# Kernel optimization log

Hardware: AMD Instinct MI355X
Metric: run time of the kernel (lower is better)

Reference implementation:

```python
import jax, jax.numpy as jnp
import numpy as np

# 4D convolution via lax.conv_general_dilated with 4 spatial dims.
# Layout: input (N, C, D, H, W, T), kernel (O, I, d, h, w, t).
DN = ('NCDHWT', 'OIDHWT', 'NCDHWT')


def conv4d(x, w, b, pad):
    # torch Conv2d/Conv4d is cross-correlation, matching lax.conv_general_dilated
    y = jax.lax.conv_general_dilated(
        x, w, window_strides=(1, 1, 1, 1),
        padding=[(pad, pad)] * 4, dimension_numbers=DN)
    return y + b.reshape(1, -1, 1, 1, 1, 1)


def _kaiming(key, shape):
    fan_out = shape[0] * int(np.prod(shape[2:]))
    std = np.sqrt(2.0 / fan_out)
    return (jax.random.normal(key, shape, dtype=jnp.float32) * std).astype(jnp.float32)


def setup_inputs() -> dict:
    key = jax.random.key(0)
    ks = jax.random.split(key, 11)
    B, W, H = 256, 16, 16
    corr = jax.random.normal(ks[0], (B, W * H, W, H), dtype=jnp.float32)
    w1 = _kaiming(ks[1], (1, 1, 17, 17, 9, 9))
    w2 = _kaiming(ks[2], (1, 1, 7, 7, 7, 7))
    w3 = _kaiming(ks[3], (1, 1, 5, 5, 5, 5))
    w4 = _kaiming(ks[4], (1, 1, 3, 3, 3, 3))
    w5 = _kaiming(ks[5], (1, 1, 8, 8, 1, 1))
    b1 = jax.random.normal(ks[6], (1,), dtype=jnp.float32) * 0.01
    b2 = jax.random.normal(ks[7], (1,), dtype=jnp.float32) * 0.01
    b3 = jax.random.normal(ks[8], (1,), dtype=jnp.float32) * 0.01
    b4 = jax.random.normal(ks[9], (1,), dtype=jnp.float32) * 0.01
    b5 = jax.random.normal(ks[10], (1,), dtype=jnp.float32) * 0.01
    return {"corr": corr, "w1": w1, "b1": b1, "w2": w2, "b2": b2,
            "w3": w3, "b3": b3, "w4": w4, "b4": b4, "w5": w5, "b5": b5}


def reference(corr, w1, b1, w2, b2, w3, b3, w4, b4, w5, b5):
    B, HW, W, H = corr.shape
    x = corr.reshape(B, 1, W, H, W, H)          # (B,1,16,16,16,16)
    x = jax.nn.relu(conv4d(x, w1, b1, 4))       # (B,1, 8, 8,16,16)
    x = jax.nn.relu(conv4d(x, w2, b2, 3))
    x = jax.nn.relu(conv4d(x, w3, b3, 2))
    x = jax.nn.relu(conv4d(x, w4, b4, 1))
    out = jax.nn.sigmoid(conv4d(x, w5, b5, 0))  # (B,1, 1, 1,16,16)
    return out.reshape(B, 1, W, H)
```

## Files before the change

### kernel.cpp

```cpp
#include <hip/hip_runtime.h>
#include <math.h>


typedef short bf16x8 __attribute__((ext_vector_type(8)));
typedef float f32x4 __attribute__((ext_vector_type(4)));
typedef unsigned int u32x4 __attribute__((ext_vector_type(4)));

#define XTS 72

__device__ __forceinline__ unsigned short f2bf(float f) {
  unsigned int u = __float_as_uint(f);
  u += 0x7fffu + ((u >> 16) & 1u);
  return (unsigned short)(u >> 16);
}

template <int KSZ, int PAD>
__device__ __forceinline__ void build_mid(const float* __restrict__ w,
                                          unsigned short* __restrict__ Bg, int gid) {
  const int lane = gid & 63;
  const int n_tile = (gid >> 6) & 3;
  const int chunk = (gid >> 8) & 1;
  const int tap = gid >> 9;
  const int kw = tap / KSZ, kt = tap - kw * KSZ;
  const int dh_o = n_tile * 16 + (lane & 15);
  const int d_o = dh_o >> 3, h_o = dh_o & 7;
  const int kbase = chunk * 32 + (lane >> 4) * 8;
  unsigned int pk[4];
#pragma unroll
  for (int p = 0; p < 4; ++p) {
    unsigned short half[2];
#pragma unroll
    for (int s = 0; s < 2; ++s) {
      const int k = kbase + p * 2 + s;
      const int d_i = k >> 3, h_i = k & 7;
      const int kd = d_i - d_o + PAD, kh = h_i - h_o + PAD;
      float v = 0.f;
      if (kd >= 0 && kd < KSZ && kh >= 0 && kh < KSZ)
        v = w[((kd * KSZ + kh) * KSZ + kw) * KSZ + kt];
      half[s] = f2bf(v);
    }
    pk[p] = (unsigned int)half[0] | ((unsigned int)half[1] << 16);
  }
  *(int4*)(Bg + (size_t)gid * 8) = make_int4(pk[0], pk[1], pk[2], pk[3]);
}

__global__ __launch_bounds__(256) void build_all(const float* __restrict__ w1,
                                                 const float* __restrict__ w2,
                                                 const float* __restrict__ w3,
                                                 const float* __restrict__ w4,
                                                 unsigned short* __restrict__ Bg1,
                                                 unsigned short* __restrict__ Bg2,
                                                 unsigned short* __restrict__ Bg3,
                                                 unsigned short* __restrict__ Bg4) {
  const int bid = blockIdx.x, tid = threadIdx.x;
  if (bid < 648) {
    const int gid = bid * 256 + tid;
    const int lane = gid & 63;
    const int n_tile = (gid >> 6) & 3;
    const int chunk = (gid >> 8) & 7;
    const int kwkt = gid >> 11;
    const int kw = kwkt / 9, kt = kwkt - kw * 9;
    const int dh_o = n_tile * 16 + (lane & 15);
    const int d_o = dh_o >> 3, h_o = dh_o & 7;
    const int kbase = chunk * 32 + (lane >> 4) * 8;
    unsigned int pk[4];
#pragma unroll
    for (int p = 0; p < 4; ++p) {
      unsigned short half[2];
#pragma unroll
      for (int s = 0; s < 2; ++s) {
        const int k = kbase + p * 2 + s;
        const int d_i = k >> 4, h_i = k & 15;
        const int kd = d_i - d_o + 4, kh = h_i - h_o + 4;
        float v = 0.f;
        if (kd >= 0 && kd < 17 && kh >= 0 && kh < 17)
          v = w1[((kd * 17 + kh) * 9 + kw) * 9 + kt];
        half[s] = f2bf(v);
      }
      pk[p] = (unsigned int)half[0] | ((unsigned int)half[1] << 16);
    }
    *(int4*)(Bg1 + (size_t)gid * 8) = make_int4(pk[0], pk[1], pk[2], pk[3]);
  } else if (bid < 746) {
    build_mid<7, 3>(w2, Bg2, (bid - 648) * 256 + tid);
  } else if (bid < 796) {
    build_mid<5, 2>(w3, Bg3, (bid - 746) * 256 + tid);
  } else {
    build_mid<3, 1>(w4, Bg4, (bid - 796) * 256 + tid);
  }
}

__device__ __forceinline__ void l1_load_tap(const unsigned short* XT,
                                            const unsigned short* __restrict__ Bg,
                                            int chbase, int kwkt, int wave, int lane,
                                            int quad, int tl, bf16x8 (&A)[8], bf16x8 (&B)[8]) {
  const int kw = kwkt / 9, kt = kwkt - kw * 9;
  const int t_i = tl + kt - 4;
  const bool tv = (unsigned)t_i < 16u;
  int ro[4];
#pragma unroll
  for (int m = 0; m < 4; ++m) {
    const int w_i = wave * 4 + m + kw - 4;
    const bool v = tv && ((unsigned)w_i < 16u);
    const int row = v ? (w_i * 16 + t_i) : 256;
    ro[m] = row * XTS + quad * 8;
  }
#pragma unroll
  for (int c = 0; c < 2; ++c)
#pragma unroll
    for (int m = 0; m < 4; ++m)
      A[c * 4 + m] = *(const bf16x8*)&XT[ro[m] + c * 32];
#pragma unroll
  for (int c = 0; c < 2; ++c)
#pragma unroll
    for (int n = 0; n < 4; ++n)
      B[c * 4 + n] = *(const bf16x8*)(Bg + (((size_t)(kwkt * 8 + chbase + c) * 4 + n) << 9) +
                                      lane * 8);
}

__device__ __forceinline__ void mfma16(const bf16x8 (&A)[8], const bf16x8 (&B)[8],
                                       f32x4 (&acc)[4][4]) {
#pragma unroll
  for (int c = 0; c < 2; ++c)
#pragma unroll
    for (int m = 0; m < 4; ++m)
#pragma unroll
      for (int n = 0; n < 4; ++n)
        acc[m][n] = __builtin_amdgcn_mfma_f32_16x16x32_bf16(A[c * 4 + m], B[c * 4 + n],
                                                            acc[m][n], 0, 0, 0);
}

__global__ __launch_bounds__(256) void conv_l1_mfma(const float* __restrict__ x,
                                                    const unsigned short* __restrict__ Bg,
                                                    float* __restrict__ P) {
  __shared__ __align__(16) unsigned short XT[257 * XTS];
  const int bx = blockIdx.x;
  const int b = bx >> 1, khalf = bx & 1;
  const int tid = threadIdx.x;
  const int lane = tid & 63, wave = tid >> 6;
  const int quad = lane >> 4, tl = lane & 15;
  const float* xb = x + (size_t)b * 65536;
  f32x4 acc[4][4] = {};

  if (tid < 9) *(int4*)&XT[256 * XTS + tid * 8] = make_int4(0, 0, 0, 0);

  for (int qq = 0; qq < 2; ++qq) {
    const int q = khalf * 2 + qq;
    __syncthreads();
#pragma unroll
    for (int it = 0; it < 8; ++it) {
      const int i = tid + it * 256;
      const int dhp = i >> 6, wtq = i & 63;
      const float4 r0 = *(const float4*)(xb + (size_t)(q * 64 + 2 * dhp) * 256 + wtq * 4);
      const float4 r1 = *(const float4*)(xb + (size_t)(q * 64 + 2 * dhp + 1) * 256 + wtq * 4);
      const float a0[4] = {r0.x, r0.y, r0.z, r0.w};
      const float a1[4] = {r1.x, r1.y, r1.z, r1.w};
#pragma unroll
      for (int j = 0; j < 4; ++j) {
        const unsigned int p = (unsigned int)f2bf(a0[j]) | ((unsigned int)f2bf(a1[j]) << 16);
        *(unsigned int*)&XT[(wtq * 4 + j) * XTS + dhp * 2] = p;
      }
    }
    __syncthreads();
    const int chbase = q * 2;
    {
      bf16x8 A0[8], B0[8], A1[8], B1[8];
      l1_load_tap(XT, Bg, chbase, 0, wave, lane, quad, tl, A0, B0);
      int k = 0;
      while (true) {
        if (k + 1 < 81) l1_load_tap(XT, Bg, chbase, k + 1, wave, lane, quad, tl, A1, B1);
        mfma16(A0, B0, acc);
        if (++k >= 81) break;
        if (k + 1 < 81) l1_load_tap(XT, Bg, chbase, k + 1, wave, lane, quad, tl, A0, B0);
        mfma16(A1, B1, acc);
        if (++k >= 81) break;
      }
    }
  }

  float* Pb = P + (size_t)(khalf * 256 + b) * 16384;
#pragma unroll
  for (int m = 0; m < 4; ++m)
#pragma unroll
    for (int n = 0; n < 4; ++n) {
      const int dh_o = n * 16 + tl;
      const int wt0 = wave * 64 + m * 16 + quad * 4;
      *(float4*)&Pb[(size_t)dh_o * 256 + wt0] = *(const float4*)&acc[m][n];
    }
}

template <int KSZ, int PAD>
__device__ __forceinline__ void tail_load_tap(const unsigned short* XT,
                                              const unsigned short* __restrict__ Bg, int kwkt,
                                              int mw, int nh, int lane, int quad, int tl,
                                              bf16x8 (&A)[8], bf16x8 (&B)[4]) {
  const int kw = kwkt / KSZ, kt = kwkt - kw * KSZ;
  const int t_i = tl + kt - PAD;
  const bool tv = (unsigned)t_i < 16u;
  int ro[4];
#pragma unroll
  for (int m = 0; m < 4; ++m) {
    const int w_i = mw * 4 + m + kw - PAD;
    const bool v = tv && ((unsigned)w_i < 16u);
    const int row = v ? (w_i * 16 + t_i) : 256;
    ro[m] = row * XTS + quad * 8;
  }
#pragma unroll
  for (int c = 0; c < 2; ++c)
#pragma unroll
    for (int m = 0; m < 4; ++m)
      A[c * 4 + m] = *(const bf16x8*)&XT[ro[m] + c * 32];
#pragma unroll
  for (int c = 0; c < 2; ++c)
#pragma unroll
    for (int n = 0; n < 2; ++n)
      B[c * 2 + n] =
          *(const bf16x8*)(Bg + (((size_t)(kwkt * 2 + c) * 4 + (nh * 2 + n)) << 9) + lane * 8);
}

__device__ __forceinline__ void mfma8(const bf16x8 (&A)[8], const bf16x8 (&B)[4],
                                      f32x4 (&acc)[4][2]) {
#pragma unroll
  for (int c = 0; c < 2; ++c)
#pragma unroll
    for (int m = 0; m < 4; ++m)
#pragma unroll
      for (int n = 0; n < 2; ++n)
        acc[m][n] = __builtin_amdgcn_mfma_f32_16x16x32_bf16(A[c * 4 + m], B[c * 2 + n],
                                                            acc[m][n], 0, 0, 0);
}

template <int KSZ, int PAD, int NT>
__device__ __forceinline__ void run_layer(unsigned short* XT,
                                          const unsigned short* __restrict__ Bg,
                                          const float bias, int mw, int nh, int lane,
                                          int quad, int tl) {
  f32x4 acc[4][2] = {};
  {
    bf16x8 A0[8], B0[4], A1[8], B1[4];
    tail_load_tap<KSZ, PAD>(XT, Bg, 0, mw, nh, lane, quad, tl, A0, B0);
    int k = 0;
    while (true) {
      if (k + 1 < NT) tail_load_tap<KSZ, PAD>(XT, Bg, k + 1, mw, nh, lane, quad, tl, A1, B1);
      mfma8(A0, B0, acc);
      if (++k >= NT) break;
      if (k + 1 < NT) tail_load_tap<KSZ, PAD>(XT, Bg, k + 1, mw, nh, lane, quad, tl, A0, B0);
      mfma8(A1, B1, acc);
      if (++k >= NT) break;
    }
  }
  __syncthreads();
#pragma unroll
  for (int m = 0; m < 4; ++m)
#pragma unroll
    for (int n = 0; n < 2; ++n) {
      const int col = (nh * 2 + n) * 16 + tl;
      const int wt0 = mw * 64 + m * 16 + quad * 4;
#pragma unroll
      for (int j = 0; j < 4; ++j)
        XT[(wt0 + j) * XTS + col] = f2bf(fmaxf(acc[m][n][j] + bias, 0.f));
    }
  __syncthreads();
}

__global__ __launch_bounds__(512) void tail_fused(const float* __restrict__ P,
                                                  const unsigned short* __restrict__ Bg2,
                                                  const unsigned short* __restrict__ Bg3,
                                                  const unsigned short* __restrict__ Bg4,
                                                  const float* __restrict__ b1,
                                                  const float* __restrict__ b2,
                                                  const float* __restrict__ b3,
                                                  const float* __restrict__ b4,
                                                  const float* __restrict__ w5,
                                                  const float* __restrict__ b5,
                                                  float* __restrict__ out) {
  __shared__ __align__(16) unsigned short XT[257 * XTS];
  const int b = blockIdx.x;
  const int tid = threadIdx.x;
  const int lane = tid & 63, wave = tid >> 6;
  const int quad = lane >> 4, tl = lane & 15;
  const int mw = wave >> 1, nh = wave & 1;
  const float* p0 = P + (size_t)b * 16384;
  const float* p1 = p0 + (size_t)256 * 16384;
  const float bias1 = b1[0];

  if (tid < 9) *(int4*)&XT[256 * XTS + tid * 8] = make_int4(0, 0, 0, 0);
#pragma unroll
  for (int it = 0; it < 4; ++it) {
    const int i = tid + it * 512;
    const int dhp = i >> 6, wtq = i & 63;
    const float* s0 = p0 + (size_t)(2 * dhp) * 256 + wtq * 4;
    const float* s1 = p1 + (size_t)(2 * dhp) * 256 + wtq * 4;
    const float4 r0a = *(const float4*)s0;
    const float4 r0b = *(const float4*)s1;
    const float4 r1a = *(const float4*)(s0 + 256);
    const float4 r1b = *(const float4*)(s1 + 256);
    float a0[4] = {r0a.x + r0b.x, r0a.y + r0b.y, r0a.z + r0b.z, r0a.w + r0b.w};
    float a1[4] = {r1a.x + r1b.x, r1a.y + r1b.y, r1a.z + r1b.z, r1a.w + r1b.w};
#pragma unroll
    for (int j = 0; j < 4; ++j) {
      const unsigned short lo = f2bf(fmaxf(a0[j] + bias1, 0.f));
      const unsigned short hi = f2bf(fmaxf(a1[j] + bias1, 0.f));
      const unsigned int p = (unsigned int)lo | ((unsigned int)hi << 16);
      *(unsigned int*)&XT[(wtq * 4 + j) * XTS + dhp * 2] = p;
    }
  }
  __syncthreads();

  run_layer<7, 3, 49>(XT, Bg2, b2[0], mw, nh, lane, quad, tl);
  run_layer<5, 2, 25>(XT, Bg3, b3[0], mw, nh, lane, quad, tl);
  run_layer<3, 1, 9>(XT, Bg4, b4[0], mw, nh, lane, quad, tl);

  if (tid < 256) {
    const int wt = tid;
    float s = b5[0];
    const unsigned short* row = &XT[wt * XTS];
#pragma unroll
    for (int k8 = 0; k8 < 8; ++k8) {
      const u32x4 v = *(const u32x4*)&row[k8 * 8];
      const unsigned int uu[4] = {(unsigned int)v.x, (unsigned int)v.y, (unsigned int)v.z,
                                  (unsigned int)v.w};
#pragma unroll
      for (int p = 0; p < 4; ++p) {
        const float lo = __uint_as_float(uu[p] << 16);
        const float hi = __uint_as_float(uu[p] & 0xFFFF0000u);
        s += lo * w5[k8 * 8 + p * 2] + hi * w5[k8 * 8 + p * 2 + 1];
      }
    }
    out[(size_t)b * 256 + wt] = 1.f / (1.f + expf(-s));
  }
}

extern "C" void kernel_launch(void* const* d_in, const int* in_sizes, int n_in,
                              void* d_out, int out_size, void* d_ws, size_t ws_size,
                              hipStream_t stream) {
  const float* corr = (const float*)d_in[0];
  const float* w1 = (const float*)d_in[1];
  const float* b1 = (const float*)d_in[2];
  const float* w2 = (const float*)d_in[3];
  const float* b2 = (const float*)d_in[4];
  const float* w3 = (const float*)d_in[5];
  const float* b3 = (const float*)d_in[6];
  const float* w4 = (const float*)d_in[7];
  const float* b4 = (const float*)d_in[8];
  const float* w5 = (const float*)d_in[9];
  const float* b5 = (const float*)d_in[10];

  float* P = (float*)d_ws;
  unsigned short* Bg1 = (unsigned short*)((char*)d_ws + (32u << 20));
  unsigned short* Bg2 = Bg1 + (size_t)81 * 8 * 4 * 64 * 8;
  unsigned short* Bg3 = Bg2 + (size_t)49 * 2 * 4 * 64 * 8;
  unsigned short* Bg4 = Bg3 + (size_t)25 * 2 * 4 * 64 * 8;

  build_all<<<814, 256, 0, stream>>>(w1, w2, w3, w4, Bg1, Bg2, Bg3, Bg4);
  conv_l1_mfma<<<512, 256, 0, stream>>>(corr, Bg1, P);
  tail_fused<<<256, 512, 0, stream>>>(P, Bg2, Bg3, Bg4, b1, b2, b3, b4, w5, b5,
                                      (float*)d_out);
}
```

Baseline: 298.4 us.

## Split layer-1 K into four partial blocks and double tail threads

```diff
diff --git a/kernel.cpp b/kernel.cpp
--- a/kernel.cpp
+++ b/kernel.cpp
@@ -89,44 +89,35 @@
   }
 }
 
-__device__ __forceinline__ void l1_load_tap(const unsigned short* XT,
-                                            const unsigned short* __restrict__ Bg,
-                                            int chbase, int kwkt, int wave, int lane,
-                                            int quad, int tl, bf16x8 (&A)[8], bf16x8 (&B)[8]) {
+__device__ __forceinline__ void l1_load_step(const unsigned short* XT,
+                                             const unsigned short* __restrict__ Bg,
+                                             int chbase, int s, int wave, int lane,
+                                             int quad, int tl, bf16x8 (&A)[4],
+                                             bf16x8 (&B)[4]) {
+  const int kwkt = s >> 1, c = s & 1;
   const int kw = kwkt / 9, kt = kwkt - kw * 9;
   const int t_i = tl + kt - 4;
   const bool tv = (unsigned)t_i < 16u;
-  int ro[4];
 #pragma unroll
   for (int m = 0; m < 4; ++m) {
     const int w_i = wave * 4 + m + kw - 4;
     const bool v = tv && ((unsigned)w_i < 16u);
     const int row = v ? (w_i * 16 + t_i) : 256;
-    ro[m] = row * XTS + quad * 8;
-  }
-#pragma unroll
-  for (int c = 0; c < 2; ++c)
-#pragma unroll
-    for (int m = 0; m < 4; ++m)
-      A[c * 4 + m] = *(const bf16x8*)&XT[ro[m] + c * 32];
-#pragma unroll
-  for (int c = 0; c < 2; ++c)
+    A[m] = *(const bf16x8*)&XT[row * XTS + quad * 8 + c * 32];
+  }
+#pragma unroll
+  for (int n = 0; n < 4; ++n)
+    B[n] = *(const bf16x8*)(Bg + (((size_t)(kwkt * 8 + chbase + c) * 4 + n) << 9) +
+                            lane * 8);
+}
+
+__device__ __forceinline__ void mfma4x4(const bf16x8 (&A)[4], const bf16x8 (&B)[4],
+                                        f32x4 (&acc)[4][4]) {
+#pragma unroll
+  for (int m = 0; m < 4; ++m)
 #pragma unroll
     for (int n = 0; n < 4; ++n)
-      B[c * 4 + n] = *(const bf16x8*)(Bg + (((size_t)(kwkt * 8 + chbase + c) * 4 + n) << 9) +
-                                      lane * 8);
-}
-
-__device__ __forceinline__ void mfma16(const bf16x8 (&A)[8], const bf16x8 (&B)[8],
-                                       f32x4 (&acc)[4][4]) {
-#pragma unroll
-  for (int c = 0; c < 2; ++c)
-#pragma unroll
-    for (int m = 0; m < 4; ++m)
-#pragma unroll
-      for (int n = 0; n < 4; ++n)
-        acc[m][n] = __builtin_amdgcn_mfma_f32_16x16x32_bf16(A[c * 4 + m], B[c * 4 + n],
-                                                            acc[m][n], 0, 0, 0);
+      acc[m][n] = __builtin_amdgcn_mfma_f32_16x16x32_bf16(A[m], B[n], acc[m][n], 0, 0, 0);
 }
 
 __global__ __launch_bounds__(256) void conv_l1_mfma(const float* __restrict__ x,
@@ -134,7 +125,7 @@
                                                     float* __restrict__ P) {
   __shared__ __align__(16) unsigned short XT[257 * XTS];
   const int bx = blockIdx.x;
-  const int b = bx >> 1, khalf = bx & 1;
+  const int b = bx >> 2, q = bx & 3;
   const int tid = threadIdx.x;
   const int lane = tid & 63, wave = tid >> 6;
   const int quad = lane >> 4, tl = lane & 15;
@@ -143,41 +134,38 @@
 
   if (tid < 9) *(int4*)&XT[256 * XTS + tid * 8] = make_int4(0, 0, 0, 0);
 
-  for (int qq = 0; qq < 2; ++qq) {
-    const int q = khalf * 2 + qq;
-    __syncthreads();
-#pragma unroll
-    for (int it = 0; it < 8; ++it) {
-      const int i = tid + it * 256;
-      const int dhp = i >> 6, wtq = i & 63;
-      const float4 r0 = *(const float4*)(xb + (size_t)(q * 64 + 2 * dhp) * 256 + wtq * 4);
-      const float4 r1 = *(const float4*)(xb + (size_t)(q * 64 + 2 * dhp + 1) * 256 + wtq * 4);
-      const float a0[4] = {r0.x, r0.y, r0.z, r0.w};
-      const float a1[4] = {r1.x, r1.y, r1.z, r1.w};
-#pragma unroll
-      for (int j = 0; j < 4; ++j) {
-        const unsigned int p = (unsigned int)f2bf(a0[j]) | ((unsigned int)f2bf(a1[j]) << 16);
-        *(unsigned int*)&XT[(wtq * 4 + j) * XTS + dhp * 2] = p;
-      }
-    }
-    __syncthreads();
-    const int chbase = q * 2;
-    {
-      bf16x8 A0[8], B0[8], A1[8], B1[8];
-      l1_load_tap(XT, Bg, chbase, 0, wave, lane, quad, tl, A0, B0);
-      int k = 0;
-      while (true) {
-        if (k + 1 < 81) l1_load_tap(XT, Bg, chbase, k + 1, wave, lane, quad, tl, A1, B1);
-        mfma16(A0, B0, acc);
-        if (++k >= 81) break;
-        if (k + 1 < 81) l1_load_tap(XT, Bg, chbase, k + 1, wave, lane, quad, tl, A0, B0);
-        mfma16(A1, B1, acc);
-        if (++k >= 81) break;
-      }
-    }
-  }
-
-  float* Pb = P + (size_t)(khalf * 256 + b) * 16384;
+#pragma unroll
+  for (int it = 0; it < 8; ++it) {
+    const int i = tid + it * 256;
+    const int dhp = i >> 6, wtq = i & 63;
+    const float4 r0 = *(const float4*)(xb + (size_t)(q * 64 + 2 * dhp) * 256 + wtq * 4);
+    const float4 r1 = *(const float4*)(xb + (size_t)(q * 64 + 2 * dhp + 1) * 256 + wtq * 4);
+    const float a0[4] = {r0.x, r0.y, r0.z, r0.w};
+    const float a1[4] = {r1.x, r1.y, r1.z, r1.w};
+#pragma unroll
+    for (int j = 0; j < 4; ++j) {
+      const unsigned int p = (unsigned int)f2bf(a0[j]) | ((unsigned int)f2bf(a1[j]) << 16);
+      *(unsigned int*)&XT[(wtq * 4 + j) * XTS + dhp * 2] = p;
+    }
+  }
+  __syncthreads();
+
+  const int chbase = q * 2;
+  {
+    bf16x8 A0[4], B0[4], A1[4], B1[4];
+    l1_load_step(XT, Bg, chbase, 0, wave, lane, quad, tl, A0, B0);
+    int s = 0;
+    while (true) {
+      if (s + 1 < 162) l1_load_step(XT, Bg, chbase, s + 1, wave, lane, quad, tl, A1, B1);
+      mfma4x4(A0, B0, acc);
+      if (++s >= 162) break;
+      if (s + 1 < 162) l1_load_step(XT, Bg, chbase, s + 1, wave, lane, quad, tl, A0, B0);
+      mfma4x4(A1, B1, acc);
+      if (++s >= 162) break;
+    }
+  }
+
+  float* Pb = P + (size_t)(q * 256 + b) * 16384;
 #pragma unroll
   for (int m = 0; m < 4; ++m)
 #pragma unroll
@@ -189,44 +177,34 @@
 }
 
 template <int KSZ, int PAD>
-__device__ __forceinline__ void tail_load_tap(const unsigned short* XT,
-                                              const unsigned short* __restrict__ Bg, int kwkt,
-                                              int mw, int nh, int lane, int quad, int tl,
-                                              bf16x8 (&A)[8], bf16x8 (&B)[4]) {
+__device__ __forceinline__ void tail_load_step(const unsigned short* XT,
+                                               const unsigned short* __restrict__ Bg,
+                                               int s, int mw, int nh, int lane, int quad,
+                                               int tl, bf16x8 (&A)[2], bf16x8 (&B)[2]) {
+  const int kwkt = s >> 1, c = s & 1;
   const int kw = kwkt / KSZ, kt = kwkt - kw * KSZ;
   const int t_i = tl + kt - PAD;
   const bool tv = (unsigned)t_i < 16u;
-  int ro[4];
-#pragma unroll
-  for (int m = 0; m < 4; ++m) {
-    const int w_i = mw * 4 + m + kw - PAD;
+#pragma unroll
+  for (int m = 0; m < 2; ++m) {
+    const int w_i = mw * 2 + m + kw - PAD;
     const bool v = tv && ((unsigned)w_i < 16u);
     const int row = v ? (w_i * 16 + t_i) : 256;
-    ro[m] = row * XTS + quad * 8;
-  }
-#pragma unroll
-  for (int c = 0; c < 2; ++c)
-#pragma unroll
-    for (int m = 0; m < 4; ++m)
-      A[c * 4 + m] = *(const bf16x8*)&XT[ro[m] + c * 32];
-#pragma unroll
-  for (int c = 0; c < 2; ++c)
+    A[m] = *(const bf16x8*)&XT[row * XTS + quad * 8 + c * 32];
+  }
+#pragma unroll
+  for (int n = 0; n < 2; ++n)
+    B[n] = *(const bf16x8*)(Bg + (((size_t)(kwkt * 2 + c) * 4 + (nh * 2 + n)) << 9) +
+                            lane * 8);
+}
+
+__device__ __forceinline__ void mfma2x2(const bf16x8 (&A)[2], const bf16x8 (&B)[2],
+                                        f32x4 (&acc)[2][2]) {
+#pragma unroll
+  for (int m = 0; m < 2; ++m)
 #pragma unroll
     for (int n = 0; n < 2; ++n)
-      B[c * 2 + n] =
-          *(const bf16x8*)(Bg + (((size_t)(kwkt * 2 + c) * 4 + (nh * 2 + n)) << 9) + lane * 8);
-}
-
-__device__ __forceinline__ void mfma8(const bf16x8 (&A)[8], const bf16x8 (&B)[4],
-                                      f32x4 (&acc)[4][2]) {
-#pragma unroll
-  for (int c = 0; c < 2; ++c)
-#pragma unroll
-    for (int m = 0; m < 4; ++m)
-#pragma unroll
-      for (int n = 0; n < 2; ++n)
-        acc[m][n] = __builtin_amdgcn_mfma_f32_16x16x32_bf16(A[c * 4 + m], B[c * 2 + n],
-                                                            acc[m][n], 0, 0, 0);
+      acc[m][n] = __builtin_amdgcn_mfma_f32_16x16x32_bf16(A[m], B[n], acc[m][n], 0, 0, 0);
 }
 
 template <int KSZ, int PAD, int NT>
@@ -234,27 +212,28 @@
                                           const unsigned short* __restrict__ Bg,
                                           const float bias, int mw, int nh, int lane,
                                           int quad, int tl) {
-  f32x4 acc[4][2] = {};
+  f32x4 acc[2][2] = {};
+  constexpr int NS = NT * 2;
   {
-    bf16x8 A0[8], B0[4], A1[8], B1[4];
-    tail_load_tap<KSZ, PAD>(XT, Bg, 0, mw, nh, lane, quad, tl, A0, B0);
-    int k = 0;
+    bf16x8 A0[2], B0[2], A1[2], B1[2];
+    tail_load_step<KSZ, PAD>(XT, Bg, 0, mw, nh, lane, quad, tl, A0, B0);
+    int s = 0;
     while (true) {
-      if (k + 1 < NT) tail_load_tap<KSZ, PAD>(XT, Bg, k + 1, mw, nh, lane, quad, tl, A1, B1);
-      mfma8(A0, B0, acc);
-      if (++k >= NT) break;
-      if (k + 1 < NT) tail_load_tap<KSZ, PAD>(XT, Bg, k + 1, mw, nh, lane, quad, tl, A0, B0);
-      mfma8(A1, B1, acc);
-      if (++k >= NT) break;
+      if (s + 1 < NS) tail_load_step<KSZ, PAD>(XT, Bg, s + 1, mw, nh, lane, quad, tl, A1, B1);
+      mfma2x2(A0, B0, acc);
+      if (++s >= NS) break;
+      if (s + 1 < NS) tail_load_step<KSZ, PAD>(XT, Bg, s + 1, mw, nh, lane, quad, tl, A0, B0);
+      mfma2x2(A1, B1, acc);
+      if (++s >= NS) break;
     }
   }
   __syncthreads();
 #pragma unroll
-  for (int m = 0; m < 4; ++m)
+  for (int m = 0; m < 2; ++m)
 #pragma unroll
     for (int n = 0; n < 2; ++n) {
       const int col = (nh * 2 + n) * 16 + tl;
-      const int wt0 = mw * 64 + m * 16 + quad * 4;
+      const int wt0 = mw * 32 + m * 16 + quad * 4;
 #pragma unroll
       for (int j = 0; j < 4; ++j)
         XT[(wt0 + j) * XTS + col] = f2bf(fmaxf(acc[m][n][j] + bias, 0.f));
@@ -262,17 +241,17 @@
   __syncthreads();
 }
 
-__global__ __launch_bounds__(512) void tail_fused(const float* __restrict__ P,
-                                                  const unsigned short* __restrict__ Bg2,
-                                                  const unsigned short* __restrict__ Bg3,
-                                                  const unsigned short* __restrict__ Bg4,
-                                                  const float* __restrict__ b1,
-                                                  const float* __restrict__ b2,
-                                                  const float* __restrict__ b3,
-                                                  const float* __restrict__ b4,
-                                                  const float* __restrict__ w5,
-                                                  const float* __restrict__ b5,
-                                                  float* __restrict__ out) {
+__global__ __launch_bounds__(1024) void tail_fused(const float* __restrict__ P,
+                                                   const unsigned short* __restrict__ Bg2,
+                                                   const unsigned short* __restrict__ Bg3,
+                                                   const unsigned short* __restrict__ Bg4,
+                                                   const float* __restrict__ b1,
+                                                   const float* __restrict__ b2,
+                                                   const float* __restrict__ b3,
+                                                   const float* __restrict__ b4,
+                                                   const float* __restrict__ w5,
+                                                   const float* __restrict__ b5,
+                                                   float* __restrict__ out) {
   __shared__ __align__(16) unsigned short XT[257 * XTS];
   const int b = blockIdx.x;
   const int tid = threadIdx.x;
@@ -281,21 +260,28 @@
   const int mw = wave >> 1, nh = wave & 1;
   const float* p0 = P + (size_t)b * 16384;
   const float* p1 = p0 + (size_t)256 * 16384;
+  const float* p2 = p0 + (size_t)512 * 16384;
+  const float* p3 = p0 + (size_t)768 * 16384;
   const float bias1 = b1[0];
 
   if (tid < 9) *(int4*)&XT[256 * XTS + tid * 8] = make_int4(0, 0, 0, 0);
 #pragma unroll
-  for (int it = 0; it < 4; ++it) {
-    const int i = tid + it * 512;
+  for (int it = 0; it < 2; ++it) {
+    const int i = tid + it * 1024;
     const int dhp = i >> 6, wtq = i & 63;
-    const float* s0 = p0 + (size_t)(2 * dhp) * 256 + wtq * 4;
-    const float* s1 = p1 + (size_t)(2 * dhp) * 256 + wtq * 4;
-    const float4 r0a = *(const float4*)s0;
-    const float4 r0b = *(const float4*)s1;
-    const float4 r1a = *(const float4*)(s0 + 256);
-    const float4 r1b = *(const float4*)(s1 + 256);
-    float a0[4] = {r0a.x + r0b.x, r0a.y + r0b.y, r0a.z + r0b.z, r0a.w + r0b.w};
-    float a1[4] = {r1a.x + r1b.x, r1a.y + r1b.y, r1a.z + r1b.z, r1a.w + r1b.w};
+    const size_t off0 = (size_t)(2 * dhp) * 256 + wtq * 4;
+    const float4 r0a = *(const float4*)(p0 + off0);
+    const float4 r0b = *(const float4*)(p1 + off0);
+    const float4 r0c = *(const float4*)(p2 + off0);
+    const float4 r0d = *(const float4*)(p3 + off0);
+    const float4 r1a = *(const float4*)(p0 + off0 + 256);
+    const float4 r1b = *(const float4*)(p1 + off0 + 256);
+    const float4 r1c = *(const float4*)(p2 + off0 + 256);
+    const float4 r1d = *(const float4*)(p3 + off0 + 256);
+    float a0[4] = {r0a.x + r0b.x + r0c.x + r0d.x, r0a.y + r0b.y + r0c.y + r0d.y,
+                   r0a.z + r0b.z + r0c.z + r0d.z, r0a.w + r0b.w + r0c.w + r0d.w};
+    float a1[4] = {r1a.x + r1b.x + r1c.x + r1d.x, r1a.y + r1b.y + r1c.y + r1d.y,
+                   r1a.z + r1b.z + r1c.z + r1d.z, r1a.w + r1b.w + r1c.w + r1d.w};
 #pragma unroll
     for (int j = 0; j < 4; ++j) {
       const unsigned short lo = f2bf(fmaxf(a0[j] + bias1, 0.f));
@@ -346,13 +332,13 @@
   const float* b5 = (const float*)d_in[10];
 
   float* P = (float*)d_ws;
-  unsigned short* Bg1 = (unsigned short*)((char*)d_ws + (32u << 20));
+  unsigned short* Bg1 = (unsigned short*)((char*)d_ws + (64u << 20));
   unsigned short* Bg2 = Bg1 + (size_t)81 * 8 * 4 * 64 * 8;
   unsigned short* Bg3 = Bg2 + (size_t)49 * 2 * 4 * 64 * 8;
   unsigned short* Bg4 = Bg3 + (size_t)25 * 2 * 4 * 64 * 8;
 
   build_all<<<814, 256, 0, stream>>>(w1, w2, w3, w4, Bg1, Bg2, Bg3, Bg4);
-  conv_l1_mfma<<<512, 256, 0, stream>>>(corr, Bg1, P);
-  tail_fused<<<256, 512, 0, stream>>>(P, Bg2, Bg3, Bg4, b1, b2, b3, b4, w5, b5,
-                                      (float*)d_out);
-}
+  conv_l1_mfma<<<1024, 256, 0, stream>>>(corr, Bg1, P);
+  tail_fused<<<256, 1024, 0, stream>>>(P, Bg2, Bg3, Bg4, b1, b2, b3, b4, w5, b5,
+                                       (float*)d_out);
+}
```

After: 325.3 us. +9.0%, slower.

## Split layer-1 conv four ways and use padded LDS rows to drop bounds checks

Applied to the files above, without the earlier changes.

```diff
diff --git a/kernel.cpp b/kernel.cpp
--- a/kernel.cpp
+++ b/kernel.cpp
@@ -7,6 +7,8 @@
 typedef unsigned int u32x4 __attribute__((ext_vector_type(4)));
 
 #define XTS 72
+#define NROWS 408
+#define ZROW 384
 
 __device__ __forceinline__ unsigned short f2bf(float f) {
   unsigned int u = __float_as_uint(f);
@@ -89,95 +91,75 @@
   }
 }
 
-__device__ __forceinline__ void l1_load_tap(const unsigned short* XT,
-                                            const unsigned short* __restrict__ Bg,
-                                            int chbase, int kwkt, int wave, int lane,
-                                            int quad, int tl, bf16x8 (&A)[8], bf16x8 (&B)[8]) {
-  const int kw = kwkt / 9, kt = kwkt - kw * 9;
-  const int t_i = tl + kt - 4;
-  const bool tv = (unsigned)t_i < 16u;
-  int ro[4];
-#pragma unroll
-  for (int m = 0; m < 4; ++m) {
-    const int w_i = wave * 4 + m + kw - 4;
-    const bool v = tv && ((unsigned)w_i < 16u);
-    const int row = v ? (w_i * 16 + t_i) : 256;
-    ro[m] = row * XTS + quad * 8;
-  }
-#pragma unroll
-  for (int c = 0; c < 2; ++c)
-#pragma unroll
-    for (int m = 0; m < 4; ++m)
-      A[c * 4 + m] = *(const bf16x8*)&XT[ro[m] + c * 32];
-#pragma unroll
-  for (int c = 0; c < 2; ++c)
-#pragma unroll
-    for (int n = 0; n < 4; ++n)
-      B[c * 4 + n] = *(const bf16x8*)(Bg + (((size_t)(kwkt * 8 + chbase + c) * 4 + n) << 9) +
-                                      lane * 8);
-}
-
-__device__ __forceinline__ void mfma16(const bf16x8 (&A)[8], const bf16x8 (&B)[8],
-                                       f32x4 (&acc)[4][4]) {
-#pragma unroll
-  for (int c = 0; c < 2; ++c)
-#pragma unroll
-    for (int m = 0; m < 4; ++m)
-#pragma unroll
-      for (int n = 0; n < 4; ++n)
-        acc[m][n] = __builtin_amdgcn_mfma_f32_16x16x32_bf16(A[c * 4 + m], B[c * 4 + n],
-                                                            acc[m][n], 0, 0, 0);
-}
-
 __global__ __launch_bounds__(256) void conv_l1_mfma(const float* __restrict__ x,
                                                     const unsigned short* __restrict__ Bg,
                                                     float* __restrict__ P) {
-  __shared__ __align__(16) unsigned short XT[257 * XTS];
+  __shared__ __align__(16) unsigned short XT[NROWS * XTS];
   const int bx = blockIdx.x;
-  const int b = bx >> 1, khalf = bx & 1;
+  const int b = bx >> 2, q = bx & 3;
   const int tid = threadIdx.x;
   const int lane = tid & 63, wave = tid >> 6;
   const int quad = lane >> 4, tl = lane & 15;
   const float* xb = x + (size_t)b * 65536;
   f32x4 acc[4][4] = {};
 
-  if (tid < 9) *(int4*)&XT[256 * XTS + tid * 8] = make_int4(0, 0, 0, 0);
-
-  for (int qq = 0; qq < 2; ++qq) {
-    const int q = khalf * 2 + qq;
-    __syncthreads();
-#pragma unroll
-    for (int it = 0; it < 8; ++it) {
-      const int i = tid + it * 256;
-      const int dhp = i >> 6, wtq = i & 63;
-      const float4 r0 = *(const float4*)(xb + (size_t)(q * 64 + 2 * dhp) * 256 + wtq * 4);
-      const float4 r1 = *(const float4*)(xb + (size_t)(q * 64 + 2 * dhp + 1) * 256 + wtq * 4);
-      const float a0[4] = {r0.x, r0.y, r0.z, r0.w};
-      const float a1[4] = {r1.x, r1.y, r1.z, r1.w};
-#pragma unroll
-      for (int j = 0; j < 4; ++j) {
-        const unsigned int p = (unsigned int)f2bf(a0[j]) | ((unsigned int)f2bf(a1[j]) << 16);
-        *(unsigned int*)&XT[(wtq * 4 + j) * XTS + dhp * 2] = p;
-      }
-    }
-    __syncthreads();
-    const int chbase = q * 2;
-    {
-      bf16x8 A0[8], B0[8], A1[8], B1[8];
-      l1_load_tap(XT, Bg, chbase, 0, wave, lane, quad, tl, A0, B0);
-      int k = 0;
-      while (true) {
-        if (k + 1 < 81) l1_load_tap(XT, Bg, chbase, k + 1, wave, lane, quad, tl, A1, B1);
-        mfma16(A0, B0, acc);
-        if (++k >= 81) break;
-        if (k + 1 < 81) l1_load_tap(XT, Bg, chbase, k + 1, wave, lane, quad, tl, A0, B0);
-        mfma16(A1, B1, acc);
-        if (++k >= 81) break;
-      }
-    }
-  }
-
-  float* Pb = P + (size_t)(khalf * 256 + b) * 16384;
+  for (int j = tid; j < (NROWS * XTS) / 8; j += 256)
+    *(int4*)&XT[j * 8] = make_int4(0, 0, 0, 0);
+  __syncthreads();
+
+#pragma unroll
+  for (int it = 0; it < 8; ++it) {
+    const int i = tid + it * 256;
+    const int dhp = i >> 6, wtq = i & 63;
+    const int r0 = (wtq >> 2) * 24 + (wtq & 3) * 4 + 4;
+    const float4 ra = *(const float4*)(xb + (size_t)(q * 64 + 2 * dhp) * 256 + wtq * 4);
+    const float4 rb = *(const float4*)(xb + (size_t)(q * 64 + 2 * dhp + 1) * 256 + wtq * 4);
+    const float a0[4] = {ra.x, ra.y, ra.z, ra.w};
+    const float a1[4] = {rb.x, rb.y, rb.z, rb.w};
+#pragma unroll
+    for (int j = 0; j < 4; ++j) {
+      const unsigned int p = (unsigned int)f2bf(a0[j]) | ((unsigned int)f2bf(a1[j]) << 16);
+      *(unsigned int*)&XT[(r0 + j) * XTS + dhp * 2] = p;
+    }
+  }
+  __syncthreads();
+
+  const int chbase = q * 2;
+  const unsigned short* Bt = Bg + (size_t)chbase * 2048 + lane * 8;
+  for (int kw = 0; kw < 9; ++kw) {
+    int ab[4];
+#pragma unroll
+    for (int m = 0; m < 4; ++m) {
+      const int w_i = wave * 4 + m + kw - 4;
+      const int rb = ((unsigned)w_i < 16u ? w_i * 24 : ZROW) + tl;
+      ab[m] = rb * XTS + quad * 8;
+    }
+#pragma unroll
+    for (int kt = 0; kt < 9; ++kt) {
+      bf16x8 A[8], B[8];
+#pragma unroll
+      for (int c = 0; c < 2; ++c)
+#pragma unroll
+        for (int m = 0; m < 4; ++m)
+          A[c * 4 + m] = *(const bf16x8*)&XT[ab[m] + kt * XTS + c * 32];
+#pragma unroll
+      for (int c = 0; c < 2; ++c)
+#pragma unroll
+        for (int n = 0; n < 4; ++n)
+          B[c * 4 + n] = *(const bf16x8*)(Bt + (size_t)kt * 16384 + c * 2048 + n * 512);
+#pragma unroll
+      for (int c = 0; c < 2; ++c)
+#pragma unroll
+        for (int m = 0; m < 4; ++m)
+#pragma unroll
+          for (int n = 0; n < 4; ++n)
+            acc[m][n] = __builtin_amdgcn_mfma_f32_16x16x32_bf16(A[c * 4 + m], B[c * 4 + n],
+                                                                acc[m][n], 0, 0, 0);
+    }
+    Bt += 9 * 16384;
+  }
+
+  float* Pb = P + (size_t)(q * 256 + b) * 16384;
 #pragma unroll
   for (int m = 0; m < 4; ++m)
 #pragma unroll
@@ -189,76 +171,57 @@
 }
 
 template <int KSZ, int PAD>
-__device__ __forceinline__ void tail_load_tap(const unsigned short* XT,
-                                              const unsigned short* __restrict__ Bg, int kwkt,
-                                              int mw, int nh, int lane, int quad, int tl,
-                                              bf16x8 (&A)[8], bf16x8 (&B)[4]) {
-  const int kw = kwkt / KSZ, kt = kwkt - kw * KSZ;
-  const int t_i = tl + kt - PAD;
-  const bool tv = (unsigned)t_i < 16u;
-  int ro[4];
-#pragma unroll
-  for (int m = 0; m < 4; ++m) {
-    const int w_i = mw * 4 + m + kw - PAD;
-    const bool v = tv && ((unsigned)w_i < 16u);
-    const int row = v ? (w_i * 16 + t_i) : 256;
-    ro[m] = row * XTS + quad * 8;
-  }
-#pragma unroll
-  for (int c = 0; c < 2; ++c)
-#pragma unroll
-    for (int m = 0; m < 4; ++m)
-      A[c * 4 + m] = *(const bf16x8*)&XT[ro[m] + c * 32];
-#pragma unroll
-  for (int c = 0; c < 2; ++c)
-#pragma unroll
-    for (int n = 0; n < 2; ++n)
-      B[c * 2 + n] =
-          *(const bf16x8*)(Bg + (((size_t)(kwkt * 2 + c) * 4 + (nh * 2 + n)) << 9) + lane * 8);
-}
-
-__device__ __forceinline__ void mfma8(const bf16x8 (&A)[8], const bf16x8 (&B)[4],
-                                      f32x4 (&acc)[4][2]) {
-#pragma unroll
-  for (int c = 0; c < 2; ++c)
-#pragma unroll
-    for (int m = 0; m < 4; ++m)
-#pragma unroll
-      for (int n = 0; n < 2; ++n)
-        acc[m][n] = __builtin_amdgcn_mfma_f32_16x16x32_bf16(A[c * 4 + m], B[c * 2 + n],
-                                                            acc[m][n], 0, 0, 0);
-}
-
-template <int KSZ, int PAD, int NT>
 __device__ __forceinline__ void run_layer(unsigned short* XT,
                                           const unsigned short* __restrict__ Bg,
                                           const float bias, int mw, int nh, int lane,
                                           int quad, int tl) {
   f32x4 acc[4][2] = {};
-  {
-    bf16x8 A0[8], B0[4], A1[8], B1[4];
-    tail_load_tap<KSZ, PAD>(XT, Bg, 0, mw, nh, lane, quad, tl, A0, B0);
-    int k = 0;
-    while (true) {
-      if (k + 1 < NT) tail_load_tap<KSZ, PAD>(XT, Bg, k + 1, mw, nh, lane, quad, tl, A1, B1);
-      mfma8(A0, B0, acc);
-      if (++k >= NT) break;
-      if (k + 1 < NT) tail_load_tap<KSZ, PAD>(XT, Bg, k + 1, mw, nh, lane, quad, tl, A0, B0);
-      mfma8(A1, B1, acc);
-      if (++k >= NT) break;
-    }
-  }
-  __syncthreads();
-#pragma unroll
-  for (int m = 0; m < 4; ++m)
+  const unsigned short* Bt = Bg + lane * 8;
+  for (int kw = 0; kw < KSZ; ++kw) {
+    int ab[4];
+#pragma unroll
+    for (int m = 0; m < 4; ++m) {
+      const int w_i = mw * 4 + m + kw - PAD;
+      const int rb = ((unsigned)w_i < 16u ? w_i * 24 : ZROW) + tl + (4 - PAD);
+      ab[m] = rb * XTS + quad * 8;
+    }
+#pragma unroll
+    for (int kt = 0; kt < KSZ; ++kt) {
+      bf16x8 A[8], B[4];
+#pragma unroll
+      for (int c = 0; c < 2; ++c)
+#pragma unroll
+        for (int m = 0; m < 4; ++m)
+          A[c * 4 + m] = *(const bf16x8*)&XT[ab[m] + kt * XTS + c * 32];
+#pragma unroll
+      for (int c = 0; c < 2; ++c)
+#pragma unroll
+        for (int n = 0; n < 2; ++n)
+          B[c * 2 + n] =
+              *(const bf16x8*)(Bt + (size_t)kt * 4096 + c * 2048 + (nh * 2 + n) * 512);
+#pragma unroll
+      for (int c = 0; c < 2; ++c)
+#pragma unroll
+        for (int m = 0; m < 4; ++m)
+#pragma unroll
+          for (int n = 0; n < 2; ++n)
+            acc[m][n] = __builtin_amdgcn_mfma_f32_16x16x32_bf16(A[c * 4 + m], B[c * 2 + n],
+                                                                acc[m][n], 0, 0, 0);
+    }
+    Bt += (size_t)KSZ * 4096;
+  }
+  __syncthreads();
+#pragma unroll
+  for (int m = 0; m < 4; ++m) {
+    const int rbase = (mw * 4 + m) * 24 + quad * 4 + 4;
 #pragma unroll
     for (int n = 0; n < 2; ++n) {
       const int col = (nh * 2 + n) * 16 + tl;
-      const int wt0 = mw * 64 + m * 16 + quad * 4;
 #pragma unroll
       for (int j = 0; j < 4; ++j)
-        XT[(wt0 + j) * XTS + col] = f2bf(fmaxf(acc[m][n][j] + bias, 0.f));
-    }
+        XT[(rbase + j) * XTS + col] = f2bf(fmaxf(acc[m][n][j] + bias, 0.f));
+    }
+  }
   __syncthreads();
 }
 
@@ -273,7 +236,7 @@
                                                   const float* __restrict__ w5,
                                                   const float* __restrict__ b5,
                                                   float* __restrict__ out) {
-  __shared__ __align__(16) unsigned short XT[257 * XTS];
+  __shared__ __align__(16) unsigned short XT[NROWS * XTS];
   const int b = blockIdx.x;
   const int tid = threadIdx.x;
   const int lane = tid & 63, wave = tid >> 6;
@@ -281,39 +244,51 @@
   const int mw = wave >> 1, nh = wave & 1;
   const float* p0 = P + (size_t)b * 16384;
   const float* p1 = p0 + (size_t)256 * 16384;
+  const float* p2 = p0 + (size_t)512 * 16384;
+  const float* p3 = p0 + (size_t)768 * 16384;
   const float bias1 = b1[0];
 
-  if (tid < 9) *(int4*)&XT[256 * XTS + tid * 8] = make_int4(0, 0, 0, 0);
+  for (int j = tid; j < (NROWS * XTS) / 8; j += 512)
+    *(int4*)&XT[j * 8] = make_int4(0, 0, 0, 0);
+  __syncthreads();
+
 #pragma unroll
   for (int it = 0; it < 4; ++it) {
     const int i = tid + it * 512;
     const int dhp = i >> 6, wtq = i & 63;
-    const float* s0 = p0 + (size_t)(2 * dhp) * 256 + wtq * 4;
-    const float* s1 = p1 + (size_t)(2 * dhp) * 256 + wtq * 4;
-    const float4 r0a = *(const float4*)s0;
-    const float4 r0b = *(const float4*)s1;
-    const float4 r1a = *(const float4*)(s0 + 256);
-    const float4 r1b = *(const float4*)(s1 + 256);
-    float a0[4] = {r0a.x + r0b.x, r0a.y + r0b.y, r0a.z + r0b.z, r0a.w + r0b.w};
-    float a1[4] = {r1a.x + r1b.x, r1a.y + r1b.y, r1a.z + r1b.z, r1a.w + r1b.w};
+    const int r0 = (wtq >> 2) * 24 + (wtq & 3) * 4 + 4;
+    const size_t off0 = (size_t)(2 * dhp) * 256 + wtq * 4;
+    const float4 r0a = *(const float4*)(p0 + off0);
+    const float4 r0b = *(const float4*)(p1 + off0);
+    const float4 r0c = *(const float4*)(p2 + off0);
+    const float4 r0d = *(const float4*)(p3 + off0);
+    const float4 r1a = *(const float4*)(p0 + off0 + 256);
+    const float4 r1b = *(const float4*)(p1 + off0 + 256);
+    const float4 r1c = *(const float4*)(p2 + off0 + 256);
+    const float4 r1d = *(const float4*)(p3 + off0 + 256);
+    float a0[4] = {r0a.x + r0b.x + r0c.x + r0d.x, r0a.y + r0b.y + r0c.y + r0d.y,
+                   r0a.z + r0b.z + r0c.z + r0d.z, r0a.w + r0b.w + r0c.w + r0d.w};
+    float a1[4] = {r1a.x + r1b.x + r1c.x + r1d.x, r1a.y + r1b.y + r1c.y + r1d.y,
+                   r1a.z + r1b.z + r1c.z + r1d.z, r1a.w + r1b.w + r1c.w + r1d.w};
 #pragma unroll
     for (int j = 0; j < 4; ++j) {
       const unsigned short lo = f2bf(fmaxf(a0[j] + bias1, 0.f));
       const unsigned short hi = f2bf(fmaxf(a1[j] + bias1, 0.f));
       const unsigned int p = (unsigned int)lo | ((unsigned int)hi << 16);
-      *(unsigned int*)&XT[(wtq * 4 + j) * XTS + dhp * 2] = p;
-    }
-  }
-  __syncthreads();
-
-  run_layer<7, 3, 49>(XT, Bg2, b2[0], mw, nh, lane, quad, tl);
-  run_layer<5, 2, 25>(XT, Bg3, b3[0], mw, nh, lane, quad, tl);
-  run_layer<3, 1, 9>(XT, Bg4, b4[0], mw, nh, lane, quad, tl);
+      *(unsigned int*)&XT[(r0 + j) * XTS + dhp * 2] = p;
+    }
+  }
+  __syncthreads();
+
+  run_layer<7, 3>(XT, Bg2, b2[0], mw, nh, lane, quad, tl);
+  run_layer<5, 2>(XT, Bg3, b3[0], mw, nh, lane, quad, tl);
+  run_layer<3, 1>(XT, Bg4, b4[0], mw, nh, lane, quad, tl);
 
   if (tid < 256) {
     const int wt = tid;
+    const int r = (wt >> 4) * 24 + (wt & 15) + 4;
     float s = b5[0];
-    const unsigned short* row = &XT[wt * XTS];
+    const unsigned short* row = &XT[r * XTS];
 #pragma unroll
     for (int k8 = 0; k8 < 8; ++k8) {
       const u32x4 v = *(const u32x4*)&row[k8 * 8];
@@ -346,13 +321,13 @@
   const float* b5 = (const float*)d_in[10];
 
   float* P = (float*)d_ws;
-  unsigned short* Bg1 = (unsigned short*)((char*)d_ws + (32u << 20));
+  unsigned short* Bg1 = (unsigned short*)((char*)d_ws + (64u << 20));
   unsigned short* Bg2 = Bg1 + (size_t)81 * 8 * 4 * 64 * 8;
   unsigned short* Bg3 = Bg2 + (size_t)49 * 2 * 4 * 64 * 8;
   unsigned short* Bg4 = Bg3 + (size_t)25 * 2 * 4 * 64 * 8;
 
   build_all<<<814, 256, 0, stream>>>(w1, w2, w3, w4, Bg1, Bg2, Bg3, Bg4);
-  conv_l1_mfma<<<512, 256, 0, stream>>>(corr, Bg1, P);
+  conv_l1_mfma<<<1024, 256, 0, stream>>>(corr, Bg1, P);
   tail_fused<<<256, 512, 0, stream>>>(P, Bg2, Bg3, Bg4, b1, b2, b3, b4, w5, b5,
                                       (float*)d_out);
 }
```

Result: slower. 313.4 us (+5.0%).
